# Performance work log

Measured on AMD Instinct MI355X. Metric: run time of the kernel, lower is better.

The kernel has to match this reference:

```python
import jax, jax.numpy as jnp
import numpy as np

N, M, D_M, D_S = 200000, 100000, 128, 128


def setup_inputs() -> dict:
    key = jax.random.key(0)
    ks = jax.random.split(key, 7)
    messages = jax.random.normal(ks[0], (M, D_M), dtype=jnp.float32)
    S = jax.random.normal(ks[1], (N, D_S), dtype=jnp.float32)
    # torch GRUCell default init: U(-1/sqrt(d_s), 1/sqrt(d_s))
    bound = 1.0 / np.sqrt(D_S)
    W_ih = jax.random.uniform(ks[2], (3 * D_S, D_M), minval=-bound, maxval=bound, dtype=jnp.float32)
    W_hh = jax.random.uniform(ks[3], (3 * D_S, D_S), minval=-bound, maxval=bound, dtype=jnp.float32)
    b_ih = jax.random.uniform(ks[4], (3 * D_S,), minval=-bound, maxval=bound, dtype=jnp.float32)
    b_hh = jax.random.uniform(ks[5], (3 * D_S,), minval=-bound, maxval=bound, dtype=jnp.float32)
    # dict keys are unique -> draw M unique node indices
    idx = jax.random.permutation(ks[6], N)[:M].astype(jnp.int64)
    return {"messages": messages, "S": S, "W_ih": W_ih, "W_hh": W_hh,
            "b_ih": b_ih, "b_hh": b_hh, "idx": idx}


def gru_cell(x, h, W_ih, W_hh, b_ih, b_hh):
    # torch.nn.GRUCell math, gate order (r, z, n)
    gi = x @ W_ih.T + b_ih          # [M, 3*d_s]
    gh = h @ W_hh.T + b_hh          # [M, 3*d_s]
    gi_r, gi_z, gi_n = jnp.split(gi, 3, axis=-1)
    gh_r, gh_z, gh_n = jnp.split(gh, 3, axis=-1)
    r = jax.nn.sigmoid(gi_r + gh_r)
    z = jax.nn.sigmoid(gi_z + gh_z)
    n = jnp.tanh(gi_n + r * gh_n)
    return (1.0 - z) * n + z * h


def reference(messages, S, W_ih, W_hh, b_ih, b_hh, idx):
    h = S[idx]                                     # gather [M, d_s]
    h_new = gru_cell(messages, h, W_ih, W_hh, b_ih, b_hh)
    # original initializes S_next = ones_like(S), then scatters updates
    return jnp.ones_like(S).at[idx].set(h_new)
```

## Files before the change

### kernel.cpp

```cpp
#include <hip/hip_runtime.h>
#include <hip/hip_bf16.h>
#include <stdint.h>

#define MM 100000
#define NN 200000
#define DD 128
#define BM 64

typedef __attribute__((ext_vector_type(8))) short short8;
typedef __attribute__((ext_vector_type(4))) float f32x4;
typedef __attribute__((ext_vector_type(4))) unsigned short u16x4;

__device__ __forceinline__ unsigned short f2bf(float f) {
    union { float f; uint32_t u; } v; v.f = f;
    return (unsigned short)((v.u + 0x7FFFu + ((v.u >> 16) & 1u)) >> 16);
}
__device__ __forceinline__ float bf2f(unsigned short s) {
    union { uint32_t u; float f; } v; v.u = ((uint32_t)s) << 16;
    return v.f;
}
__device__ __forceinline__ float sigmoidf(float x) {
    return 1.0f / (1.0f + __expf(-x));
}
__device__ __forceinline__ float tanh_fast(float x) {
    return 2.0f / (1.0f + __expf(-2.0f * x)) - 1.0f;
}

__global__ void fill_ones(f32x4* __restrict__ out, int n4) {
    int i = blockIdx.x * blockDim.x + threadIdx.x;
    int stride = gridDim.x * blockDim.x;
    f32x4 ones = {1.f, 1.f, 1.f, 1.f};
    for (; i < n4; i += stride) out[i] = ones;
}

__global__ void conv_w(const float* __restrict__ wih, const float* __restrict__ whh,
                       unsigned short* __restrict__ dst) {
    int i = blockIdx.x * blockDim.x + threadIdx.x;
    if (i < 3 * DD * DD) {
        dst[i] = f2bf(wih[i]);
        dst[3 * DD * DD + i] = f2bf(whh[i]);
    }
}

template <bool WBF16>
__device__ __forceinline__ short8 load_wfrag(const void* W, int row, int kbase) {
    if constexpr (WBF16) {
        const unsigned short* p = (const unsigned short*)W;
        return *reinterpret_cast<const short8*>(p + (size_t)row * DD + kbase);
    } else {
        const float* p = (const float*)W + (size_t)row * DD + kbase;
        f32x4 a = *reinterpret_cast<const f32x4*>(p);
        f32x4 b = *reinterpret_cast<const f32x4*>(p + 4);
        short8 r;
        r[0] = (short)f2bf(a[0]); r[1] = (short)f2bf(a[1]);
        r[2] = (short)f2bf(a[2]); r[3] = (short)f2bf(a[3]);
        r[4] = (short)f2bf(b[0]); r[5] = (short)f2bf(b[1]);
        r[6] = (short)f2bf(b[2]); r[7] = (short)f2bf(b[3]);
        return r;
    }
}

template <bool WBF16>
__global__ __launch_bounds__(512, 2) void gru_kernel(
    const float* __restrict__ msgs, const float* __restrict__ S,
    const void* __restrict__ Wih, const void* __restrict__ Whh,
    const float* __restrict__ b_ih, const float* __restrict__ b_hh,
    const int* __restrict__ idx, float* __restrict__ out)
{
    __shared__ unsigned short Xl[BM][136];
    __shared__ unsigned short Hl[BM][136];

    const int tid = threadIdx.x;
    const int mbase = blockIdx.x * BM;

    #pragma unroll
    for (int it = 0; it < 4; ++it) {
        int id = it * 512 + tid;
        int row = id >> 5, ch = id & 31;
        int m = mbase + row;
        f32x4 xv = {0.f, 0.f, 0.f, 0.f}, hv = {0.f, 0.f, 0.f, 0.f};
        if (m < MM) {
            xv = *reinterpret_cast<const f32x4*>(msgs + (size_t)m * DD + ch * 4);
            int si = idx[m];
            hv = *reinterpret_cast<const f32x4*>(S + (size_t)si * DD + ch * 4);
        }
        u16x4 xb, hb;
        #pragma unroll
        for (int j = 0; j < 4; ++j) { xb[j] = f2bf(xv[j]); hb[j] = f2bf(hv[j]); }
        *reinterpret_cast<u16x4*>(&Xl[row][ch * 4]) = xb;
        *reinterpret_cast<u16x4*>(&Hl[row][ch * 4]) = hb;
    }
    __syncthreads();

    const int wave = tid >> 6;
    const int lane = tid & 63;
    const int l15 = lane & 15;
    const int lk = lane >> 4;
    const int cbase = wave * 16;

    f32x4 accX[3][4], accH[3][4];
    #pragma unroll
    for (int g = 0; g < 3; ++g) {
        #pragma unroll
        for (int mt = 0; mt < 4; ++mt) {
            accX[g][mt] = (f32x4){0.f, 0.f, 0.f, 0.f};
            accH[g][mt] = (f32x4){0.f, 0.f, 0.f, 0.f};
        }
    }

    #pragma unroll
    for (int ks = 0; ks < 4; ++ks) {
        short8 ax[4], ah[4];
        #pragma unroll
        for (int mt = 0; mt < 4; ++mt) {
            ax[mt] = *reinterpret_cast<const short8*>(&Xl[mt * 16 + l15][ks * 32 + lk * 8]);
            ah[mt] = *reinterpret_cast<const short8*>(&Hl[mt * 16 + l15][ks * 32 + lk * 8]);
        }
        #pragma unroll
        for (int g = 0; g < 3; ++g) {
            int wrow = g * DD + cbase + l15;
            int kb = ks * 32 + lk * 8;
            short8 bx = load_wfrag<WBF16>(Wih, wrow, kb);
            #pragma unroll
            for (int mt = 0; mt < 4; ++mt)
                accX[g][mt] = __builtin_amdgcn_mfma_f32_16x16x32_bf16(ax[mt], bx, accX[g][mt], 0, 0, 0);
            short8 bh = load_wfrag<WBF16>(Whh, wrow, kb);
            #pragma unroll
            for (int mt = 0; mt < 4; ++mt)
                accH[g][mt] = __builtin_amdgcn_mfma_f32_16x16x32_bf16(ah[mt], bh, accH[g][mt], 0, 0, 0);
        }
    }

    const int c = cbase + l15;
    float bir = b_ih[c], biz = b_ih[DD + c], bin_ = b_ih[2 * DD + c];
    float bhr = b_hh[c], bhz = b_hh[DD + c], bhn = b_hh[2 * DD + c];
    #pragma unroll
    for (int mt = 0; mt < 4; ++mt) {
        #pragma unroll
        for (int j = 0; j < 4; ++j) {
            int mloc = mt * 16 + lk * 4 + j;
            int m = mbase + mloc;
            if (m < MM) {
                float r = sigmoidf(accX[0][mt][j] + bir + accH[0][mt][j] + bhr);
                float z = sigmoidf(accX[1][mt][j] + biz + accH[1][mt][j] + bhz);
                float n = tanh_fast(accX[2][mt][j] + bin_ + r * (accH[2][mt][j] + bhn));
                float h = bf2f(Hl[mloc][c]);
                int o = idx[m];
                out[(size_t)o * DD + c] = (1.f - z) * n + z * h;
            }
        }
    }
}

extern "C" void kernel_launch(void* const* d_in, const int* in_sizes, int n_in,
                              void* d_out, int out_size, void* d_ws, size_t ws_size,
                              hipStream_t stream) {
    const float* msgs  = (const float*)d_in[0];
    const float* S     = (const float*)d_in[1];
    const float* W_ih  = (const float*)d_in[2];
    const float* W_hh  = (const float*)d_in[3];
    const float* b_ih  = (const float*)d_in[4];
    const float* b_hh  = (const float*)d_in[5];
    const int*   idx   = (const int*)d_in[6];
    float* out = (float*)d_out;

    fill_ones<<<2048, 256, 0, stream>>>((f32x4*)out, NN * DD / 4);

    const int blocks = (MM + BM - 1) / BM;
    const size_t wbytes = (size_t)2 * 3 * DD * DD * sizeof(unsigned short);
    if (ws_size >= wbytes) {
        unsigned short* wbf = (unsigned short*)d_ws;
        conv_w<<<(3 * DD * DD + 255) / 256, 256, 0, stream>>>(W_ih, W_hh, wbf);
        gru_kernel<true><<<blocks, 512, 0, stream>>>(msgs, S, wbf, wbf + 3 * DD * DD,
                                                     b_ih, b_hh, idx, out);
    } else {
        gru_kernel<false><<<blocks, 512, 0, stream>>>(msgs, S, W_ih, W_hh,
                                                      b_ih, b_hh, idx, out);
    }
}
```

Baseline: 297.6 us.

## Fill ones only for untouched rows and shrink GRU tile to 16 rows

Adds a byte mask built from idx so the ones fill writes only output rows that no GRU update touches, instead of writing the full output and then overwriting half of it. The GRU kernel tile drops from 64 to 16 rows per block with higher occupancy bounds. It also merges the r/z accumulators across input and hidden, pre-sums the biases, and caches the scatter indices in shared memory. This adds three small launches and a byte-mask read per float4 in the fill, and it drops the bounds check on the assumption that M divides by 16. Weight fragments are now reused across only 16 rows per load.

```diff
diff --git a/kernel.cpp b/kernel.cpp
--- a/kernel.cpp
+++ b/kernel.cpp
@@ -5,7 +5,7 @@
 #define MM 100000
 #define NN 200000
 #define DD 128
-#define BM 64
+#define BM 16
 
 typedef __attribute__((ext_vector_type(8))) short short8;
 typedef __attribute__((ext_vector_type(4))) float f32x4;
@@ -31,6 +31,24 @@
     int stride = gridDim.x * blockDim.x;
     f32x4 ones = {1.f, 1.f, 1.f, 1.f};
     for (; i < n4; i += stride) out[i] = ones;
+}
+
+__global__ void clear_mark(uint32_t* __restrict__ mark32) {
+    int i = blockIdx.x * blockDim.x + threadIdx.x;
+    if (i < NN / 4) mark32[i] = 0;
+}
+
+__global__ void mark_rows(const int* __restrict__ idx, uint8_t* __restrict__ mark) {
+    int m = blockIdx.x * blockDim.x + threadIdx.x;
+    if (m < MM) mark[idx[m]] = 1;
+}
+
+__global__ void fill_unmarked(const uint8_t* __restrict__ mark, f32x4* __restrict__ out4) {
+    int i = blockIdx.x * blockDim.x + threadIdx.x;
+    int stride = gridDim.x * blockDim.x;
+    f32x4 ones = {1.f, 1.f, 1.f, 1.f};
+    for (; i < NN * 32; i += stride)
+        if (!mark[i >> 5]) out4[i] = ones;
 }
 
 __global__ void conv_w(const float* __restrict__ wih, const float* __restrict__ whh,
@@ -61,7 +79,7 @@
 }
 
 template <bool WBF16>
-__global__ __launch_bounds__(512, 2) void gru_kernel(
+__global__ __launch_bounds__(512, 8) void gru_kernel(
     const float* __restrict__ msgs, const float* __restrict__ S,
     const void* __restrict__ Wih, const void* __restrict__ Whh,
     const float* __restrict__ b_ih, const float* __restrict__ b_hh,
@@ -69,26 +87,23 @@
 {
     __shared__ unsigned short Xl[BM][136];
     __shared__ unsigned short Hl[BM][136];
+    __shared__ int Il[BM];
 
     const int tid = threadIdx.x;
     const int mbase = blockIdx.x * BM;
 
-    #pragma unroll
-    for (int it = 0; it < 4; ++it) {
-        int id = it * 512 + tid;
-        int row = id >> 5, ch = id & 31;
+    {
+        int row = tid >> 5, ch = tid & 31;
         int m = mbase + row;
-        f32x4 xv = {0.f, 0.f, 0.f, 0.f}, hv = {0.f, 0.f, 0.f, 0.f};
-        if (m < MM) {
-            xv = *reinterpret_cast<const f32x4*>(msgs + (size_t)m * DD + ch * 4);
-            int si = idx[m];
-            hv = *reinterpret_cast<const f32x4*>(S + (size_t)si * DD + ch * 4);
-        }
+        int si = idx[m];
+        f32x4 xv = *reinterpret_cast<const f32x4*>(msgs + (size_t)m * DD + ch * 4);
+        f32x4 hv = *reinterpret_cast<const f32x4*>(S + (size_t)si * DD + ch * 4);
         u16x4 xb, hb;
         #pragma unroll
         for (int j = 0; j < 4; ++j) { xb[j] = f2bf(xv[j]); hb[j] = f2bf(hv[j]); }
         *reinterpret_cast<u16x4*>(&Xl[row][ch * 4]) = xb;
         *reinterpret_cast<u16x4*>(&Hl[row][ch * 4]) = hb;
+        if (ch == 0) Il[row] = si;
     }
     __syncthreads();
 
@@ -98,57 +113,49 @@
     const int lk = lane >> 4;
     const int cbase = wave * 16;
 
-    f32x4 accX[3][4], accH[3][4];
-    #pragma unroll
-    for (int g = 0; g < 3; ++g) {
-        #pragma unroll
-        for (int mt = 0; mt < 4; ++mt) {
-            accX[g][mt] = (f32x4){0.f, 0.f, 0.f, 0.f};
-            accH[g][mt] = (f32x4){0.f, 0.f, 0.f, 0.f};
-        }
-    }
+    f32x4 accR = {0.f, 0.f, 0.f, 0.f};
+    f32x4 accZ = {0.f, 0.f, 0.f, 0.f};
+    f32x4 accNi = {0.f, 0.f, 0.f, 0.f};
+    f32x4 accNh = {0.f, 0.f, 0.f, 0.f};
+
+    const int wrow = cbase + l15;
 
     #pragma unroll
     for (int ks = 0; ks < 4; ++ks) {
-        short8 ax[4], ah[4];
-        #pragma unroll
-        for (int mt = 0; mt < 4; ++mt) {
-            ax[mt] = *reinterpret_cast<const short8*>(&Xl[mt * 16 + l15][ks * 32 + lk * 8]);
-            ah[mt] = *reinterpret_cast<const short8*>(&Hl[mt * 16 + l15][ks * 32 + lk * 8]);
-        }
-        #pragma unroll
-        for (int g = 0; g < 3; ++g) {
-            int wrow = g * DD + cbase + l15;
-            int kb = ks * 32 + lk * 8;
-            short8 bx = load_wfrag<WBF16>(Wih, wrow, kb);
-            #pragma unroll
-            for (int mt = 0; mt < 4; ++mt)
-                accX[g][mt] = __builtin_amdgcn_mfma_f32_16x16x32_bf16(ax[mt], bx, accX[g][mt], 0, 0, 0);
-            short8 bh = load_wfrag<WBF16>(Whh, wrow, kb);
-            #pragma unroll
-            for (int mt = 0; mt < 4; ++mt)
-                accH[g][mt] = __builtin_amdgcn_mfma_f32_16x16x32_bf16(ah[mt], bh, accH[g][mt], 0, 0, 0);
-        }
+        const int kb = ks * 32 + lk * 8;
+        short8 ax = *reinterpret_cast<const short8*>(&Xl[l15][kb]);
+        short8 ah = *reinterpret_cast<const short8*>(&Hl[l15][kb]);
+
+        short8 bRi = load_wfrag<WBF16>(Wih, wrow, kb);
+        short8 bRh = load_wfrag<WBF16>(Whh, wrow, kb);
+        accR = __builtin_amdgcn_mfma_f32_16x16x32_bf16(ax, bRi, accR, 0, 0, 0);
+        accR = __builtin_amdgcn_mfma_f32_16x16x32_bf16(ah, bRh, accR, 0, 0, 0);
+
+        short8 bZi = load_wfrag<WBF16>(Wih, DD + wrow, kb);
+        short8 bZh = load_wfrag<WBF16>(Whh, DD + wrow, kb);
+        accZ = __builtin_amdgcn_mfma_f32_16x16x32_bf16(ax, bZi, accZ, 0, 0, 0);
+        accZ = __builtin_amdgcn_mfma_f32_16x16x32_bf16(ah, bZh, accZ, 0, 0, 0);
+
+        short8 bNi = load_wfrag<WBF16>(Wih, 2 * DD + wrow, kb);
+        short8 bNh = load_wfrag<WBF16>(Whh, 2 * DD + wrow, kb);
+        accNi = __builtin_amdgcn_mfma_f32_16x16x32_bf16(ax, bNi, accNi, 0, 0, 0);
+        accNh = __builtin_amdgcn_mfma_f32_16x16x32_bf16(ah, bNh, accNh, 0, 0, 0);
     }
 
     const int c = cbase + l15;
-    float bir = b_ih[c], biz = b_ih[DD + c], bin_ = b_ih[2 * DD + c];
-    float bhr = b_hh[c], bhz = b_hh[DD + c], bhn = b_hh[2 * DD + c];
+    const float br = b_ih[c] + b_hh[c];
+    const float bz = b_ih[DD + c] + b_hh[DD + c];
+    const float bin_ = b_ih[2 * DD + c];
+    const float bhn = b_hh[2 * DD + c];
     #pragma unroll
-    for (int mt = 0; mt < 4; ++mt) {
-        #pragma unroll
-        for (int j = 0; j < 4; ++j) {
-            int mloc = mt * 16 + lk * 4 + j;
-            int m = mbase + mloc;
-            if (m < MM) {
-                float r = sigmoidf(accX[0][mt][j] + bir + accH[0][mt][j] + bhr);
-                float z = sigmoidf(accX[1][mt][j] + biz + accH[1][mt][j] + bhz);
-                float n = tanh_fast(accX[2][mt][j] + bin_ + r * (accH[2][mt][j] + bhn));
-                float h = bf2f(Hl[mloc][c]);
-                int o = idx[m];
-                out[(size_t)o * DD + c] = (1.f - z) * n + z * h;
-            }
-        }
+    for (int j = 0; j < 4; ++j) {
+        int mloc = lk * 4 + j;
+        float r = sigmoidf(accR[j] + br);
+        float z = sigmoidf(accZ[j] + bz);
+        float n = tanh_fast(accNi[j] + bin_ + r * (accNh[j] + bhn));
+        float h = bf2f(Hl[mloc][c]);
+        int o = Il[mloc];
+        out[(size_t)o * DD + c] = (1.f - z) * n + z * h;
     }
 }
 
@@ -164,16 +171,21 @@
     const int*   idx   = (const int*)d_in[6];
     float* out = (float*)d_out;
 
-    fill_ones<<<2048, 256, 0, stream>>>((f32x4*)out, NN * DD / 4);
+    const int blocks = MM / BM;
+    const size_t wbytes = (size_t)2 * 3 * DD * DD * sizeof(unsigned short);
+    const size_t need = wbytes + NN + 256;
 
-    const int blocks = (MM + BM - 1) / BM;
-    const size_t wbytes = (size_t)2 * 3 * DD * DD * sizeof(unsigned short);
-    if (ws_size >= wbytes) {
+    if (ws_size >= need) {
         unsigned short* wbf = (unsigned short*)d_ws;
+        uint8_t* mark = (uint8_t*)d_ws + wbytes;
+        clear_mark<<<(NN / 4 + 511) / 512, 512, 0, stream>>>((uint32_t*)mark);
+        mark_rows<<<(MM + 511) / 512, 512, 0, stream>>>(idx, mark);
         conv_w<<<(3 * DD * DD + 255) / 256, 256, 0, stream>>>(W_ih, W_hh, wbf);
         gru_kernel<true><<<blocks, 512, 0, stream>>>(msgs, S, wbf, wbf + 3 * DD * DD,
                                                      b_ih, b_hh, idx, out);
+        fill_unmarked<<<2048, 256, 0, stream>>>(mark, (f32x4*)out);
     } else {
+        fill_ones<<<2048, 256, 0, stream>>>((f32x4*)out, NN * DD / 4);
         gru_kernel<false><<<blocks, 512, 0, stream>>>(msgs, S, W_ih, W_hh,
                                                       b_ih, b_hh, idx, out);
     }
```

Result: slower. 347.7 us (+16.8%).

## Make GRU kernel persistent with register prefetch and double-buffered LDS tiles

Applied to the files above, without the earlier changes.

Switches from one block per 64-row tile to a persistent grid of 256 blocks that loop over tiles. The next tile's messages, gathered S rows and indices are prefetched into registers while the current tile's MFMAs run, using double-buffered LDS. The r and z gate accumulators are merged across the input and hidden GEMMs and the biases are pre-summed, and scatter indices are cached in LDS. The aim is to hide gather latency and cut launch and tail costs, at the price of higher register pressure and only 256 blocks to fill the device.

```diff
diff --git a/kernel.cpp b/kernel.cpp
--- a/kernel.cpp
+++ b/kernel.cpp
@@ -6,6 +6,8 @@
 #define NN 200000
 #define DD 128
 #define BM 64
+#define NT 1563
+#define GRID 256
 
 typedef __attribute__((ext_vector_type(8))) short short8;
 typedef __attribute__((ext_vector_type(4))) float f32x4;
@@ -67,88 +69,137 @@
     const float* __restrict__ b_ih, const float* __restrict__ b_hh,
     const int* __restrict__ idx, float* __restrict__ out)
 {
-    __shared__ unsigned short Xl[BM][136];
-    __shared__ unsigned short Hl[BM][136];
+    __shared__ unsigned short Xl[2][BM][136];
+    __shared__ unsigned short Hl[2][BM][136];
+    __shared__ int Il[2][BM];
 
     const int tid = threadIdx.x;
-    const int mbase = blockIdx.x * BM;
-
-    #pragma unroll
-    for (int it = 0; it < 4; ++it) {
-        int id = it * 512 + tid;
-        int row = id >> 5, ch = id & 31;
-        int m = mbase + row;
-        f32x4 xv = {0.f, 0.f, 0.f, 0.f}, hv = {0.f, 0.f, 0.f, 0.f};
-        if (m < MM) {
-            xv = *reinterpret_cast<const f32x4*>(msgs + (size_t)m * DD + ch * 4);
-            int si = idx[m];
-            hv = *reinterpret_cast<const f32x4*>(S + (size_t)si * DD + ch * 4);
-        }
-        u16x4 xb, hb;
-        #pragma unroll
-        for (int j = 0; j < 4; ++j) { xb[j] = f2bf(xv[j]); hb[j] = f2bf(hv[j]); }
-        *reinterpret_cast<u16x4*>(&Xl[row][ch * 4]) = xb;
-        *reinterpret_cast<u16x4*>(&Hl[row][ch * 4]) = hb;
-    }
-    __syncthreads();
-
     const int wave = tid >> 6;
     const int lane = tid & 63;
     const int l15 = lane & 15;
-    const int lk = lane >> 4;
-    const int cbase = wave * 16;
-
-    f32x4 accX[3][4], accH[3][4];
+    const int lk  = lane >> 4;
+    const int c   = wave * 16 + l15;
+
+    const float br   = b_ih[c] + b_hh[c];
+    const float bz   = b_ih[DD + c] + b_hh[DD + c];
+    const float bn_i = b_ih[2 * DD + c];
+    const float bn_h = b_hh[2 * DD + c];
+
+    const int srow = tid >> 5;
+    const int sch  = tid & 31;
+
+    int t = blockIdx.x;
+
+    int si_g[4];
+    int si_n[4];
+    f32x4 px[4], ph[4];
     #pragma unroll
-    for (int g = 0; g < 3; ++g) {
+    for (int it = 0; it < 4; ++it) {
+        int m = t * BM + srow + it * 16;
+        int mm = m < MM ? m : MM - 1;
+        si_g[it] = idx[mm];
+    }
+    #pragma unroll
+    for (int it = 0; it < 4; ++it) {
+        int m = t * BM + srow + it * 16;
+        int mm = m < MM ? m : MM - 1;
+        px[it] = *reinterpret_cast<const f32x4*>(msgs + (size_t)mm * DD + sch * 4);
+        ph[it] = *reinterpret_cast<const f32x4*>(S + (size_t)si_g[it] * DD + sch * 4);
+    }
+    if (t + GRID < NT) {
+        #pragma unroll
+        for (int it = 0; it < 4; ++it) {
+            int m = (t + GRID) * BM + srow + it * 16;
+            int mm = m < MM ? m : MM - 1;
+            si_n[it] = idx[mm];
+        }
+    }
+
+    int p = 0;
+    for (; t < NT; t += GRID) {
+        const bool hasn = (t + GRID) < NT;
+
+        #pragma unroll
+        for (int it = 0; it < 4; ++it) {
+            u16x4 xb, hb;
+            #pragma unroll
+            for (int j = 0; j < 4; ++j) { xb[j] = f2bf(px[it][j]); hb[j] = f2bf(ph[it][j]); }
+            *reinterpret_cast<u16x4*>(&Xl[p][srow + it * 16][sch * 4]) = xb;
+            *reinterpret_cast<u16x4*>(&Hl[p][srow + it * 16][sch * 4]) = hb;
+            if (sch == 0) Il[p][srow + it * 16] = si_g[it];
+        }
+        __syncthreads();
+
+        if (hasn) {
+            #pragma unroll
+            for (int it = 0; it < 4; ++it) {
+                int m = (t + GRID) * BM + srow + it * 16;
+                int mm = m < MM ? m : MM - 1;
+                px[it] = *reinterpret_cast<const f32x4*>(msgs + (size_t)mm * DD + sch * 4);
+                ph[it] = *reinterpret_cast<const f32x4*>(S + (size_t)si_n[it] * DD + sch * 4);
+                si_g[it] = si_n[it];
+            }
+            if (t + 2 * GRID < NT) {
+                #pragma unroll
+                for (int it = 0; it < 4; ++it) {
+                    int m = (t + 2 * GRID) * BM + srow + it * 16;
+                    int mm = m < MM ? m : MM - 1;
+                    si_n[it] = idx[mm];
+                }
+            }
+        }
+
+        f32x4 accR[4], accZ[4], accNi[4], accNh[4];
         #pragma unroll
         for (int mt = 0; mt < 4; ++mt) {
-            accX[g][mt] = (f32x4){0.f, 0.f, 0.f, 0.f};
-            accH[g][mt] = (f32x4){0.f, 0.f, 0.f, 0.f};
-        }
-    }
-
-    #pragma unroll
-    for (int ks = 0; ks < 4; ++ks) {
-        short8 ax[4], ah[4];
+            accR[mt] = (f32x4){0.f, 0.f, 0.f, 0.f};
+            accZ[mt] = (f32x4){0.f, 0.f, 0.f, 0.f};
+            accNi[mt] = (f32x4){0.f, 0.f, 0.f, 0.f};
+            accNh[mt] = (f32x4){0.f, 0.f, 0.f, 0.f};
+        }
+        #pragma unroll
+        for (int ks = 0; ks < 4; ++ks) {
+            const int kb = ks * 32 + lk * 8;
+            short8 ax[4], ah[4];
+            #pragma unroll
+            for (int mt = 0; mt < 4; ++mt) {
+                ax[mt] = *reinterpret_cast<const short8*>(&Xl[p][mt * 16 + l15][kb]);
+                ah[mt] = *reinterpret_cast<const short8*>(&Hl[p][mt * 16 + l15][kb]);
+            }
+            short8 bRi = load_wfrag<WBF16>(Wih, c, kb);
+            short8 bRh = load_wfrag<WBF16>(Whh, c, kb);
+            short8 bZi = load_wfrag<WBF16>(Wih, DD + c, kb);
+            short8 bZh = load_wfrag<WBF16>(Whh, DD + c, kb);
+            short8 bNi = load_wfrag<WBF16>(Wih, 2 * DD + c, kb);
+            short8 bNh = load_wfrag<WBF16>(Whh, 2 * DD + c, kb);
+            #pragma unroll
+            for (int mt = 0; mt < 4; ++mt) {
+                accR[mt]  = __builtin_amdgcn_mfma_f32_16x16x32_bf16(ax[mt], bRi, accR[mt], 0, 0, 0);
+                accR[mt]  = __builtin_amdgcn_mfma_f32_16x16x32_bf16(ah[mt], bRh, accR[mt], 0, 0, 0);
+                accZ[mt]  = __builtin_amdgcn_mfma_f32_16x16x32_bf16(ax[mt], bZi, accZ[mt], 0, 0, 0);
+                accZ[mt]  = __builtin_amdgcn_mfma_f32_16x16x32_bf16(ah[mt], bZh, accZ[mt], 0, 0, 0);
+                accNi[mt] = __builtin_amdgcn_mfma_f32_16x16x32_bf16(ax[mt], bNi, accNi[mt], 0, 0, 0);
+                accNh[mt] = __builtin_amdgcn_mfma_f32_16x16x32_bf16(ah[mt], bNh, accNh[mt], 0, 0, 0);
+            }
+        }
+
+        const int mb = t * BM;
         #pragma unroll
         for (int mt = 0; mt < 4; ++mt) {
-            ax[mt] = *reinterpret_cast<const short8*>(&Xl[mt * 16 + l15][ks * 32 + lk * 8]);
-            ah[mt] = *reinterpret_cast<const short8*>(&Hl[mt * 16 + l15][ks * 32 + lk * 8]);
-        }
-        #pragma unroll
-        for (int g = 0; g < 3; ++g) {
-            int wrow = g * DD + cbase + l15;
-            int kb = ks * 32 + lk * 8;
-            short8 bx = load_wfrag<WBF16>(Wih, wrow, kb);
-            #pragma unroll
-            for (int mt = 0; mt < 4; ++mt)
-                accX[g][mt] = __builtin_amdgcn_mfma_f32_16x16x32_bf16(ax[mt], bx, accX[g][mt], 0, 0, 0);
-            short8 bh = load_wfrag<WBF16>(Whh, wrow, kb);
-            #pragma unroll
-            for (int mt = 0; mt < 4; ++mt)
-                accH[g][mt] = __builtin_amdgcn_mfma_f32_16x16x32_bf16(ah[mt], bh, accH[g][mt], 0, 0, 0);
-        }
-    }
-
-    const int c = cbase + l15;
-    float bir = b_ih[c], biz = b_ih[DD + c], bin_ = b_ih[2 * DD + c];
-    float bhr = b_hh[c], bhz = b_hh[DD + c], bhn = b_hh[2 * DD + c];
-    #pragma unroll
-    for (int mt = 0; mt < 4; ++mt) {
-        #pragma unroll
-        for (int j = 0; j < 4; ++j) {
-            int mloc = mt * 16 + lk * 4 + j;
-            int m = mbase + mloc;
-            if (m < MM) {
-                float r = sigmoidf(accX[0][mt][j] + bir + accH[0][mt][j] + bhr);
-                float z = sigmoidf(accX[1][mt][j] + biz + accH[1][mt][j] + bhz);
-                float n = tanh_fast(accX[2][mt][j] + bin_ + r * (accH[2][mt][j] + bhn));
-                float h = bf2f(Hl[mloc][c]);
-                int o = idx[m];
-                out[(size_t)o * DD + c] = (1.f - z) * n + z * h;
-            }
-        }
+            #pragma unroll
+            for (int j = 0; j < 4; ++j) {
+                int mloc = mt * 16 + lk * 4 + j;
+                int m = mb + mloc;
+                if (m < MM) {
+                    float r = sigmoidf(accR[mt][j] + br);
+                    float z = sigmoidf(accZ[mt][j] + bz);
+                    float n = tanh_fast(accNi[mt][j] + bn_i + r * (accNh[mt][j] + bn_h));
+                    float h = bf2f(Hl[p][mloc][c]);
+                    out[(size_t)Il[p][mloc] * DD + c] = (1.f - z) * n + z * h;
+                }
+            }
+        }
+        p ^= 1;
     }
 }
 
@@ -166,15 +217,14 @@
 
     fill_ones<<<2048, 256, 0, stream>>>((f32x4*)out, NN * DD / 4);
 
-    const int blocks = (MM + BM - 1) / BM;
     const size_t wbytes = (size_t)2 * 3 * DD * DD * sizeof(unsigned short);
     if (ws_size >= wbytes) {
         unsigned short* wbf = (unsigned short*)d_ws;
         conv_w<<<(3 * DD * DD + 255) / 256, 256, 0, stream>>>(W_ih, W_hh, wbf);
-        gru_kernel<true><<<blocks, 512, 0, stream>>>(msgs, S, wbf, wbf + 3 * DD * DD,
-                                                     b_ih, b_hh, idx, out);
+        gru_kernel<true><<<GRID, 512, 0, stream>>>(msgs, S, wbf, wbf + 3 * DD * DD,
+                                                   b_ih, b_hh, idx, out);
     } else {
-        gru_kernel<false><<<blocks, 512, 0, stream>>>(msgs, S, W_ih, W_hh,
-                                                      b_ih, b_hh, idx, out);
-    }
-}
+        gru_kernel<false><<<GRID, 512, 0, stream>>>(msgs, S, W_ih, W_hh,
+                                                    b_ih, b_hh, idx, out);
+    }
+}
```

Result: faster. 254.2 us (-14.6%).
